# Performance work log

Measured on AMD Instinct MI355X. Metric: run time of the kernel, lower is better.

The kernel has to match this reference:

```python
import jax, jax.numpy as jnp
import numpy as np

DIM = 768
HEADS = 12
DH = DIM // HEADS
SCALE = DH ** -0.5


def setup_inputs() -> dict:
    key = jax.random.key(0)
    ks = jax.random.split(key, 8)
    B, N = 8, 1024
    x = jax.random.normal(ks[0], (B, N, DIM), dtype=jnp.float32)
    rpb = jax.random.normal(ks[1], (1, HEADS, N, N), dtype=jnp.float32)
    s = DIM ** -0.5
    W_qkv = jax.random.normal(ks[2], (DIM, 3 * DIM), dtype=jnp.float32) * s
    W_out = jax.random.normal(ks[3], (DIM, DIM), dtype=jnp.float32) * s
    b_out = jnp.zeros((DIM,), dtype=jnp.float32)
    ln_g = jnp.ones((DIM,), dtype=jnp.float32)
    ln_b = jnp.zeros((DIM,), dtype=jnp.float32)
    return {"x": x, "relative_position_bias": rpb, "W_qkv": W_qkv,
            "W_out": W_out, "b_out": b_out, "ln_g": ln_g, "ln_b": ln_b}


def reference(x, relative_position_bias, W_qkv, W_out, b_out, ln_g, ln_b):
    # LayerNorm (eps matches torch default 1e-5)
    mu = jnp.mean(x, axis=-1, keepdims=True)
    var = jnp.mean(jnp.square(x - mu), axis=-1, keepdims=True)
    xn = (x - mu) * jax.lax.rsqrt(var + 1e-5) * ln_g + ln_b

    qkv = xn @ W_qkv                                  # [b,n,3*dim]
    q, k, v = jnp.split(qkv, 3, axis=-1)
    B, N, _ = x.shape
    reshape = lambda t: t.reshape(B, N, HEADS, DH).transpose(0, 2, 1, 3)  # b h n d
    q, k, v = reshape(q), reshape(k), reshape(v)

    scores = jnp.einsum('bhid,bhjd->bhij', q, k) * SCALE + relative_position_bias
    attn = jax.nn.softmax(scores, axis=-1)            # dropout p=0.0 -> identity
    out = jnp.einsum('bhij,bhjd->bhid', attn, v)
    out = out.transpose(0, 2, 1, 3).reshape(B, N, HEADS * DH)
    return out @ W_out + b_out
```

## Files before the change

### kernel.cpp

```cpp
#include <hip/hip_runtime.h>
#include <hip/hip_bf16.h>
#include <math.h>

#define BATCH 8
#define NSEQ  1024
#define DIMM  768
#define NHEAD 12
#define DHEAD 64
#define SCALE 0.125f
#define ROWS  (BATCH * NSEQ)
#define LOG2E 1.44269504f
#define SCALE_L2E (0.125f * 1.44269504f)

typedef __hip_bfloat16 bf16;
typedef __bf16 bf16x8 __attribute__((ext_vector_type(8)));
typedef float  f32x4  __attribute__((ext_vector_type(4)));

#if __has_builtin(__builtin_amdgcn_global_load_lds)
#define HAVE_GLL 1
typedef __attribute__((address_space(3))) void lds_void_t;
typedef const __attribute__((address_space(1))) void gbl_void_t;
__device__ __forceinline__ void gload16(const void* g, void* l) {
    __builtin_amdgcn_global_load_lds((gbl_void_t*)g, (lds_void_t*)l, 16, 0, 0);
}
#else
#define HAVE_GLL 0
#endif

__device__ __forceinline__ unsigned pk2(float a, float b) {
    union { unsigned u; bf16 h[2]; } x;
    x.h[0] = __float2bfloat16(a);
    x.h[1] = __float2bfloat16(b);
    return x.u;
}

__global__ __launch_bounds__(256) void ln_kernel(const float* __restrict__ x,
                                                 const float* __restrict__ g,
                                                 const float* __restrict__ bta,
                                                 bf16* __restrict__ y) {
    __shared__ float ps[4], pq[4];
    __shared__ float mean_s, rstd_s;
    int row = blockIdx.x;
    int tid = threadIdx.x;
    const float* xr = x + (size_t)row * DIMM;
    float v[3];
    float s = 0.f, sq = 0.f;
#pragma unroll
    for (int i = 0; i < 3; ++i) {
        v[i] = xr[tid + 256 * i];
        s += v[i];
        sq += v[i] * v[i];
    }
#pragma unroll
    for (int off = 32; off >= 1; off >>= 1) {
        s  += __shfl_down(s, off);
        sq += __shfl_down(sq, off);
    }
    int wid = tid >> 6, lane = tid & 63;
    if (lane == 0) { ps[wid] = s; pq[wid] = sq; }
    __syncthreads();
    if (tid == 0) {
        float S = ps[0] + ps[1] + ps[2] + ps[3];
        float Q = pq[0] + pq[1] + pq[2] + pq[3];
        float mean = S * (1.0f / DIMM);
        float var  = Q * (1.0f / DIMM) - mean * mean;
        mean_s = mean;
        rstd_s = rsqrtf(fmaxf(var, 0.f) + 1e-5f);
    }
    __syncthreads();
    float mean = mean_s, rstd = rstd_s;
    bf16* yr = y + (size_t)row * DIMM;
#pragma unroll
    for (int i = 0; i < 3; ++i) {
        int c = tid + 256 * i;
        yr[c] = __float2bfloat16((v[i] - mean) * rstd * g[c] + bta[c]);
    }
}

__global__ __launch_bounds__(256) void transpose_bf16(const float* __restrict__ W,
                                                      bf16* __restrict__ Wt,
                                                      int K, int N) {
    __shared__ float t[32][33];
    int n0 = blockIdx.x * 32, k0 = blockIdx.y * 32;
    int tx = threadIdx.x, ty = threadIdx.y;
#pragma unroll
    for (int i = 0; i < 32; i += 8)
        t[ty + i][tx] = W[(size_t)(k0 + ty + i) * N + n0 + tx];
    __syncthreads();
#pragma unroll
    for (int i = 0; i < 32; i += 8)
        Wt[(size_t)(n0 + ty + i) * K + k0 + tx] = __float2bfloat16(t[tx][ty + i]);
}

template <bool OUT_BF16>
__global__ __launch_bounds__(256) void gemm_mfma(const bf16* __restrict__ A,
                                                 const bf16* __restrict__ Bt,
                                                 const float* __restrict__ bias,
                                                 void* __restrict__ Cv,
                                                 int M, int Nn, int K) {
    __shared__ bf16 As[2][128][32];
    __shared__ bf16 Bs[2][128][32];
    int tid = threadIdx.x;
    int wave = tid >> 6, lane = tid & 63, quad = lane >> 4, l16 = lane & 15;
    int wm = (wave >> 1) * 64, wn = (wave & 1) * 64;
    int m0 = blockIdx.y * 128, n0 = blockIdx.x * 128;

    f32x4 acc[4][4] = {};

#if HAVE_GLL
    const char* Ag = (const char*)(A  + (size_t)(m0 + (tid >> 2)) * K + (tid & 3) * 8);
    const char* Bg = (const char*)(Bt + (size_t)(n0 + (tid >> 2)) * K + (tid & 3) * 8);
    char* AsB = (char*)&As[0][0][0] + tid * 16;
    char* BsB = (char*)&Bs[0][0][0] + tid * 16;
    const size_t radv = (size_t)64 * K * 2;

    gload16(Ag, AsB);
    gload16(Ag + radv, AsB + 4096);
    gload16(Bg, BsB);
    gload16(Bg + radv, BsB + 4096);
    Ag += 64; Bg += 64;
    __syncthreads();

    int cur = 0;
    for (int k0 = 0; k0 < K; k0 += 32) {
        int nxt = cur ^ 1;
        if (k0 + 32 < K) {
            gload16(Ag, AsB + nxt * 8192);
            gload16(Ag + radv, AsB + nxt * 8192 + 4096);
            gload16(Bg, BsB + nxt * 8192);
            gload16(Bg + radv, BsB + nxt * 8192 + 4096);
            Ag += 64; Bg += 64;
        }
#else
    int srow = tid >> 1;
    int sk = (tid & 1) * 16;
    const bf16* Ap = A  + (size_t)(m0 + srow) * K + sk;
    const bf16* Bp = Bt + (size_t)(n0 + srow) * K + sk;
    {
        uint4 a0 = *(const uint4*)(Ap);
        uint4 a1 = *(const uint4*)(Ap + 8);
        uint4 b0 = *(const uint4*)(Bp);
        uint4 b1 = *(const uint4*)(Bp + 8);
        *(uint4*)&As[0][srow][sk]     = a0;
        *(uint4*)&As[0][srow][sk + 8] = a1;
        *(uint4*)&Bs[0][srow][sk]     = b0;
        *(uint4*)&Bs[0][srow][sk + 8] = b1;
    }
    __syncthreads();
    int cur = 0;
    for (int k0 = 0; k0 < K; k0 += 32) {
        int nxt = cur ^ 1;
        uint4 a0, a1, b0, b1;
        if (k0 + 32 < K) {
            a0 = *(const uint4*)(Ap + k0 + 32);
            a1 = *(const uint4*)(Ap + k0 + 40);
            b0 = *(const uint4*)(Bp + k0 + 32);
            b1 = *(const uint4*)(Bp + k0 + 40);
        }
#endif
        bf16x8 af[4], bf_[4];
#pragma unroll
        for (int i = 0; i < 4; ++i) {
            af[i]  = *(const bf16x8*)&As[cur][wm + i * 16 + l16][quad * 8];
            bf_[i] = *(const bf16x8*)&Bs[cur][wn + i * 16 + l16][quad * 8];
        }
#pragma unroll
        for (int mi = 0; mi < 4; ++mi)
#pragma unroll
            for (int ni = 0; ni < 4; ++ni)
                acc[mi][ni] = __builtin_amdgcn_mfma_f32_16x16x32_bf16(
                    af[mi], bf_[ni], acc[mi][ni], 0, 0, 0);
#if !HAVE_GLL
        if (k0 + 32 < K) {
            *(uint4*)&As[nxt][srow][sk]     = a0;
            *(uint4*)&As[nxt][srow][sk + 8] = a1;
            *(uint4*)&Bs[nxt][srow][sk]     = b0;
            *(uint4*)&Bs[nxt][srow][sk + 8] = b1;
        }
#endif
        __syncthreads();
        cur = nxt;
    }

    float bv[4] = {0.f, 0.f, 0.f, 0.f};
    if (!OUT_BF16 && bias) {
#pragma unroll
        for (int ni = 0; ni < 4; ++ni) bv[ni] = bias[n0 + wn + ni * 16 + l16];
    }
#pragma unroll
    for (int mi = 0; mi < 4; ++mi)
#pragma unroll
        for (int reg = 0; reg < 4; ++reg) {
            size_t row = m0 + wm + mi * 16 + quad * 4 + reg;
#pragma unroll
            for (int ni = 0; ni < 4; ++ni) {
                int col = n0 + wn + ni * 16 + l16;
                float val = acc[mi][ni][reg] + bv[ni];
                if (OUT_BF16)
                    ((bf16*)Cv)[row * Nn + col] = __float2bfloat16(val);
                else
                    ((float*)Cv)[row * Nn + col] = val;
            }
        }
}

#define KTILEB (64 * 3 * DIMM * 2)
#define NBLK   (BATCH * NHEAD * (NSEQ / 64))

__global__ __launch_bounds__(256, 4) void attn_mfma(const bf16* __restrict__ qkv,
                                                    const float* __restrict__ rpb,
                                                    bf16* __restrict__ outb) {
    __shared__ char KsRaw[2][8192];
    __shared__ unsigned Vt32[64][36];
    __shared__ bf16 Ps[4][16][72];

    int tid = threadIdx.x;
    int wave = tid >> 6, lane = tid & 63, quad = lane >> 4, l16 = lane & 15;

    int p   = blockIdx.x;
    int wid = (p & 7) * (NBLK / 8) + (p >> 3);
    int h   = wid >> 7;
    int rem = wid & 127;
    int b   = rem >> 4;
    int mt  = rem & 15;
    int m0  = mt * 64;

    const bf16* qrow = qkv + (size_t)(b * NSEQ + m0 + wave * 16 + l16) * (3 * DIMM) + h * DHEAD;
    bf16x8 qf0 = *(const bf16x8*)(qrow + quad * 8);
    bf16x8 qf1 = *(const bf16x8*)(qrow + 32 + quad * 8);

    const float* rp = rpb + ((size_t)h * NSEQ + (m0 + wave * 16 + l16)) * NSEQ;

#if HAVE_GLL
    const char* kgl = (const char*)(qkv + (size_t)(b * NSEQ + wave * 16 + l16) * (3 * DIMM)
                                    + DIMM + h * DHEAD + quad * 8);
    char* kdst = &KsRaw[0][0] + tid * 16 + wave * 1024;
#else
    int ksr = tid >> 2, ksd = (tid & 3) * 16;
    const bf16* kgf = qkv + (size_t)(b * NSEQ + ksr) * (3 * DIMM) + DIMM + h * DHEAD + ksd;
#endif

    int vk = (tid >> 3) * 2;
    int vd = (tid & 7) * 8;
    int vkp = tid >> 3;
    const bf16* vg = qkv + (size_t)(b * NSEQ + vk) * (3 * DIMM) + 2 * DIMM + h * DHEAD + vd;
    int wblk = (((vkp >> 2) ^ (vd >> 3)) << 2) | (vkp & 3);

    float m_s = -INFINITY, l_s = 0.f;
    f32x4 acco[4] = {};

#if HAVE_GLL
    gload16(kgl, kdst);
    gload16(kgl + 64, kdst + 1024);
#endif
    uint4 va = *(const uint4*)(vg);
    uint4 vb = *(const uint4*)(vg + 3 * DIMM);
#if !HAVE_GLL
    {
        uint4 k0v = *(const uint4*)(kgf);
        uint4 k1v = *(const uint4*)(kgf + 8);
        char* d0 = &KsRaw[0][0] + (ksr >> 4) * 2048 + (ksd >> 5) * 1024 + ((((ksd >> 3) & 3) * 16 + (ksr & 15)) * 16);
        *(uint4*)d0 = k0v;
        char* d1 = &KsRaw[0][0] + (ksr >> 4) * 2048 + ((ksd + 8) >> 5) * 1024 + (((((ksd + 8) >> 3) & 3) * 16 + (ksr & 15)) * 16);
        *(uint4*)d1 = k1v;
    }
#endif
    {
        union { uint4 q; unsigned short u[8]; } A_, B_;
        A_.q = va; B_.q = vb;
#pragma unroll
        for (int j = 0; j < 8; ++j)
            Vt32[vd + j][wblk] = (unsigned)A_.u[j] | ((unsigned)B_.u[j] << 16);
    }
    float4 rv[4];
#pragma unroll
    for (int t = 0; t < 4; ++t) {
        float4 r = *(const float4*)&rp[t * 16 + quad * 4];
        rv[t] = make_float4(r.x * LOG2E, r.y * LOG2E, r.z * LOG2E, r.w * LOG2E);
    }
    __syncthreads();

    for (int kt = 0; kt < 16; ++kt) {
        int cur = kt & 1, nxt = cur ^ 1;

        float4 rvn[4];
        if (kt + 1 < 16) {
#if HAVE_GLL
            const char* kg2 = kgl + (size_t)(kt + 1) * KTILEB;
            gload16(kg2, kdst + nxt * 8192);
            gload16(kg2 + 64, kdst + nxt * 8192 + 1024);
#endif
            const bf16* v2 = vg + (size_t)(kt + 1) * 64 * (3 * DIMM);
            va = *(const uint4*)(v2);
            vb = *(const uint4*)(v2 + 3 * DIMM);
            const float* rpn = rp + (kt + 1) * 64;
#pragma unroll
            for (int t = 0; t < 4; ++t) {
                float4 r = *(const float4*)&rpn[t * 16 + quad * 4];
                rvn[t] = make_float4(r.x * LOG2E, r.y * LOG2E, r.z * LOG2E, r.w * LOG2E);
            }
        }

        f32x4 accs[4] = {};
        __builtin_amdgcn_s_setprio(1);
#pragma unroll
        for (int t = 0; t < 4; ++t) {
            const char* kb = &KsRaw[cur][0] + t * 2048 + (quad * 16 + l16) * 16;
            bf16x8 kf0 = *(const bf16x8*)(kb);
            bf16x8 kf1 = *(const bf16x8*)(kb + 1024);
            accs[t] = __builtin_amdgcn_mfma_f32_16x16x32_bf16(kf0, qf0, accs[t], 0, 0, 0);
            accs[t] = __builtin_amdgcn_mfma_f32_16x16x32_bf16(kf1, qf1, accs[t], 0, 0, 0);
        }
        __builtin_amdgcn_s_setprio(0);

        float mx = -INFINITY;
        {
            float rb[4][4] = {{rv[0].x, rv[0].y, rv[0].z, rv[0].w},
                              {rv[1].x, rv[1].y, rv[1].z, rv[1].w},
                              {rv[2].x, rv[2].y, rv[2].z, rv[2].w},
                              {rv[3].x, rv[3].y, rv[3].z, rv[3].w}};
#pragma unroll
            for (int t = 0; t < 4; ++t)
#pragma unroll
                for (int r = 0; r < 4; ++r) {
                    accs[t][r] = fmaf(accs[t][r], SCALE_L2E, rb[t][r]);
                    mx = fmaxf(mx, accs[t][r]);
                }
        }
        mx = fmaxf(mx, __shfl_xor(mx, 16));
        mx = fmaxf(mx, __shfl_xor(mx, 32));

        if (__any(mx > m_s + 11.5f)) {
            float mn = fmaxf(m_s, mx);
            float alpha = exp2f(m_s - mn);
            m_s = mn;
            l_s *= alpha;
            float ab[4];
#pragma unroll
            for (int r = 0; r < 4; ++r) ab[r] = __shfl(alpha, quad * 4 + r);
#pragma unroll
            for (int dt = 0; dt < 4; ++dt)
#pragma unroll
                for (int r = 0; r < 4; ++r) acco[dt][r] *= ab[r];
        }

        float sum = 0.f;
#pragma unroll
        for (int t = 0; t < 4; ++t)
#pragma unroll
            for (int r = 0; r < 4; ++r) {
                float pv = exp2f(accs[t][r] - m_s);
                accs[t][r] = pv;
                sum += pv;
            }
        sum += __shfl_xor(sum, 16);
        sum += __shfl_xor(sum, 32);
        l_s += sum;

#pragma unroll
        for (int t = 0; t < 4; ++t) {
            uint2 w;
            w.x = pk2(accs[t][0], accs[t][1]);
            w.y = pk2(accs[t][2], accs[t][3]);
            *(uint2*)&Ps[wave][l16][t * 16 + quad * 4] = w;
        }
        __asm__ volatile("s_waitcnt lgkmcnt(0)" ::: "memory");

        __builtin_amdgcn_s_setprio(1);
#pragma unroll
        for (int s = 0; s < 2; ++s) {
            bf16x8 pf = *(const bf16x8*)&Ps[wave][l16][s * 32 + quad * 8];
#pragma unroll
            for (int dt = 0; dt < 4; ++dt) {
                int row = dt * 16 + l16;
                int sblk = (((s * 4 + quad) ^ ((row >> 3) & 7)) << 2);
                bf16x8 vf = *(const bf16x8*)&Vt32[row][sblk];
                acco[dt] = __builtin_amdgcn_mfma_f32_16x16x32_bf16(pf, vf, acco[dt], 0, 0, 0);
            }
        }
        __builtin_amdgcn_s_setprio(0);

        if (kt + 1 < 16) {
            __syncthreads();
            union { uint4 q; unsigned short u[8]; } A_, B_;
            A_.q = va; B_.q = vb;
#pragma unroll
            for (int j = 0; j < 8; ++j)
                Vt32[vd + j][wblk] = (unsigned)A_.u[j] | ((unsigned)B_.u[j] << 16);
#pragma unroll
            for (int t = 0; t < 4; ++t) rv[t] = rvn[t];
            __syncthreads();
        }
    }

    float invl[4];
#pragma unroll
    for (int r = 0; r < 4; ++r) invl[r] = 1.f / __shfl(l_s, quad * 4 + r);
    bf16* orow = outb + (size_t)(b * NSEQ + m0 + wave * 16) * DIMM + h * DHEAD;
#pragma unroll
    for (int dt = 0; dt < 4; ++dt)
#pragma unroll
        for (int r = 0; r < 4; ++r)
            orow[(size_t)(quad * 4 + r) * DIMM + dt * 16 + l16] =
                __float2bfloat16(acco[dt][r] * invl[r]);
}

extern "C" void kernel_launch(void* const* d_in, const int* in_sizes, int n_in,
                              void* d_out, int out_size, void* d_ws, size_t ws_size,
                              hipStream_t stream) {
    const float* x     = (const float*)d_in[0];
    const float* rpb   = (const float*)d_in[1];
    const float* W_qkv = (const float*)d_in[2];
    const float* W_out = (const float*)d_in[3];
    const float* b_out = (const float*)d_in[4];
    const float* ln_g  = (const float*)d_in[5];
    const float* ln_b  = (const float*)d_in[6];
    float* out = (float*)d_out;

    char* p = (char*)d_ws;
    bf16* xn    = (bf16*)p; p += (size_t)ROWS * DIMM * 2;
    bf16* qkv   = (bf16*)p; p += (size_t)ROWS * 3 * DIMM * 2;
    bf16* attn  = (bf16*)p; p += (size_t)ROWS * DIMM * 2;
    bf16* WqkvT = (bf16*)p; p += (size_t)3 * DIMM * DIMM * 2;
    bf16* WoutT = (bf16*)p; p += (size_t)DIMM * DIMM * 2;

    ln_kernel<<<ROWS, 256, 0, stream>>>(x, ln_g, ln_b, xn);
    transpose_bf16<<<dim3(3 * DIMM / 32, DIMM / 32), dim3(32, 8), 0, stream>>>(
        W_qkv, WqkvT, DIMM, 3 * DIMM);
    transpose_bf16<<<dim3(DIMM / 32, DIMM / 32), dim3(32, 8), 0, stream>>>(
        W_out, WoutT, DIMM, DIMM);

    gemm_mfma<true><<<dim3(3 * DIMM / 128, ROWS / 128), 256, 0, stream>>>(
        xn, WqkvT, nullptr, qkv, ROWS, 3 * DIMM, DIMM);

    attn_mfma<<<NBLK, 256, 0, stream>>>(qkv, rpb, attn);

    gemm_mfma<false><<<dim3(DIMM / 128, ROWS / 128), 256, 0, stream>>>(
        attn, WoutT, b_out, out, ROWS, DIMM, DIMM);
}
```

Baseline: 277.7 us.

## Triple-buffer GEMM LDS loads and double-buffer V tile in attention

The GEMM main loop moves from double to triple buffering of the A/B LDS tiles. It issues loads two stages ahead and uses explicit vmcnt waits plus a single barrier per iteration instead of a full syncthreads. The attention kernel double-buffers the transposed V tile, so the next tile's write no longer needs a barrier before it, cutting two barriers per key tile to one. Both changes add LDS usage, which may lower occupancy (the attention kernel declares 4 blocks per CU), and they depend on correct manual waitcnt accounting.

```diff
diff --git a/kernel.cpp b/kernel.cpp
--- a/kernel.cpp
+++ b/kernel.cpp
@@ -98,8 +98,8 @@
                                                  const float* __restrict__ bias,
                                                  void* __restrict__ Cv,
                                                  int M, int Nn, int K) {
-    __shared__ bf16 As[2][128][32];
-    __shared__ bf16 Bs[2][128][32];
+    __shared__ bf16 As[3][128][32];
+    __shared__ bf16 Bs[3][128][32];
     int tid = threadIdx.x;
     int wave = tid >> 6, lane = tid & 63, quad = lane >> 4, l16 = lane & 15;
     int wm = (wave >> 1) * 64, wn = (wave & 1) * 64;
@@ -114,23 +114,42 @@
     char* BsB = (char*)&Bs[0][0][0] + tid * 16;
     const size_t radv = (size_t)64 * K * 2;
 
-    gload16(Ag, AsB);
-    gload16(Ag + radv, AsB + 4096);
-    gload16(Bg, BsB);
-    gload16(Bg + radv, BsB + 4096);
+    const int nt = K >> 5;
+    gload16(Ag, AsB);        gload16(Ag + radv, AsB + 4096);
+    gload16(Bg, BsB);        gload16(Bg + radv, BsB + 4096);
     Ag += 64; Bg += 64;
-    __syncthreads();
-
-    int cur = 0;
-    for (int k0 = 0; k0 < K; k0 += 32) {
-        int nxt = cur ^ 1;
-        if (k0 + 32 < K) {
-            gload16(Ag, AsB + nxt * 8192);
-            gload16(Ag + radv, AsB + nxt * 8192 + 4096);
-            gload16(Bg, BsB + nxt * 8192);
-            gload16(Bg + radv, BsB + nxt * 8192 + 4096);
+    gload16(Ag, AsB + 8192); gload16(Ag + radv, AsB + 8192 + 4096);
+    gload16(Bg, BsB + 8192); gload16(Bg + radv, BsB + 8192 + 4096);
+    Ag += 64; Bg += 64;
+
+    int cur = 0, st = 2;
+    for (int t = 0; t < nt; ++t) {
+        if (t + 1 < nt) { asm volatile("s_waitcnt vmcnt(4)" ::: "memory"); }
+        else            { asm volatile("s_waitcnt vmcnt(0)" ::: "memory"); }
+        __builtin_amdgcn_s_barrier();
+        __builtin_amdgcn_sched_barrier(0);
+        if (t + 2 < nt) {
+            char* ad = AsB + st * 8192;
+            char* bd = BsB + st * 8192;
+            gload16(Ag, ad); gload16(Ag + radv, ad + 4096);
+            gload16(Bg, bd); gload16(Bg + radv, bd + 4096);
             Ag += 64; Bg += 64;
         }
+        bf16x8 af[4], bf_[4];
+#pragma unroll
+        for (int i = 0; i < 4; ++i) {
+            af[i]  = *(const bf16x8*)&As[cur][wm + i * 16 + l16][quad * 8];
+            bf_[i] = *(const bf16x8*)&Bs[cur][wn + i * 16 + l16][quad * 8];
+        }
+#pragma unroll
+        for (int mi = 0; mi < 4; ++mi)
+#pragma unroll
+            for (int ni = 0; ni < 4; ++ni)
+                acc[mi][ni] = __builtin_amdgcn_mfma_f32_16x16x32_bf16(
+                    af[mi], bf_[ni], acc[mi][ni], 0, 0, 0);
+        cur = (cur + 1 == 3) ? 0 : cur + 1;
+        st  = (st  + 1 == 3) ? 0 : st  + 1;
+    }
 #else
     int srow = tid >> 1;
     int sk = (tid & 1) * 16;
@@ -157,7 +176,6 @@
             b0 = *(const uint4*)(Bp + k0 + 32);
             b1 = *(const uint4*)(Bp + k0 + 40);
         }
-#endif
         bf16x8 af[4], bf_[4];
 #pragma unroll
         for (int i = 0; i < 4; ++i) {
@@ -170,17 +188,16 @@
             for (int ni = 0; ni < 4; ++ni)
                 acc[mi][ni] = __builtin_amdgcn_mfma_f32_16x16x32_bf16(
                     af[mi], bf_[ni], acc[mi][ni], 0, 0, 0);
-#if !HAVE_GLL
         if (k0 + 32 < K) {
             *(uint4*)&As[nxt][srow][sk]     = a0;
             *(uint4*)&As[nxt][srow][sk + 8] = a1;
             *(uint4*)&Bs[nxt][srow][sk]     = b0;
             *(uint4*)&Bs[nxt][srow][sk + 8] = b1;
         }
-#endif
         __syncthreads();
         cur = nxt;
     }
+#endif
 
     float bv[4] = {0.f, 0.f, 0.f, 0.f};
     if (!OUT_BF16 && bias) {
@@ -211,7 +228,7 @@
                                                     const float* __restrict__ rpb,
                                                     bf16* __restrict__ outb) {
     __shared__ char KsRaw[2][8192];
-    __shared__ unsigned Vt32[64][36];
+    __shared__ unsigned Vt32[2][64][36];
     __shared__ bf16 Ps[4][16][72];
 
     int tid = threadIdx.x;
@@ -270,7 +287,7 @@
         A_.q = va; B_.q = vb;
 #pragma unroll
         for (int j = 0; j < 8; ++j)
-            Vt32[vd + j][wblk] = (unsigned)A_.u[j] | ((unsigned)B_.u[j] << 16);
+            Vt32[0][vd + j][wblk] = (unsigned)A_.u[j] | ((unsigned)B_.u[j] << 16);
     }
     float4 rv[4];
 #pragma unroll
@@ -374,23 +391,22 @@
             for (int dt = 0; dt < 4; ++dt) {
                 int row = dt * 16 + l16;
                 int sblk = (((s * 4 + quad) ^ ((row >> 3) & 7)) << 2);
-                bf16x8 vf = *(const bf16x8*)&Vt32[row][sblk];
+                bf16x8 vf = *(const bf16x8*)&Vt32[cur][row][sblk];
                 acco[dt] = __builtin_amdgcn_mfma_f32_16x16x32_bf16(pf, vf, acco[dt], 0, 0, 0);
             }
         }
         __builtin_amdgcn_s_setprio(0);
 
         if (kt + 1 < 16) {
-            __syncthreads();
             union { uint4 q; unsigned short u[8]; } A_, B_;
             A_.q = va; B_.q = vb;
 #pragma unroll
             for (int j = 0; j < 8; ++j)
-                Vt32[vd + j][wblk] = (unsigned)A_.u[j] | ((unsigned)B_.u[j] << 16);
+                Vt32[nxt][vd + j][wblk] = (unsigned)A_.u[j] | ((unsigned)B_.u[j] << 16);
 #pragma unroll
             for (int t = 0; t < 4; ++t) rv[t] = rvn[t];
-            __syncthreads();
-        }
+        }
+        __syncthreads();
     }
 
     float invl[4];
```

Result: no change. 279.5 us (+0.7%).
